# Kernel tuning notes

Hardware: AMD Instinct MI355X
Metric: run time of the kernel (lower is better)

The kernel has to match this reference:

```python
import jax, jax.numpy as jnp
import numpy as np

B, T, E, A = 4, 4096, 1024, 1024

def setup_inputs() -> dict:
    key = jax.random.key(0)
    k1, k2, k3, k4 = jax.random.split(key, 4)
    scale = 1.0 / np.sqrt(E)  # ~ nn.Linear default init scale
    return {
        "embedded": jax.random.normal(k1, (B, T, E), dtype=jnp.float32),
        "Wq": jax.random.uniform(k2, (A, E), jnp.float32, -scale, scale),
        "Wk": jax.random.uniform(k3, (A, E), jnp.float32, -scale, scale),
        "Wv": jax.random.uniform(k4, (A, E), jnp.float32, -scale, scale),
    }

def reference(embedded, Wq, Wk, Wv):
    # QKV projections (nn.Linear without bias: x @ W.T)
    q = jnp.einsum('bte,ae->bta', embedded, Wq)
    k = jnp.einsum('bte,ae->bta', embedded, Wk)
    v = jnp.einsum('bte,ae->bta', embedded, Wv)
    A_dim = q.shape[-1]
    # scaled scores [B, T, T]
    scores = jnp.einsum('bqa,bka->bqk', q, k) / jnp.sqrt(jnp.float32(A_dim))
    # causal mask (lower triangular allowed)
    Tq = scores.shape[-1]
    causal = jnp.tril(jnp.ones((Tq, Tq), dtype=bool))
    scores = jnp.where(causal, scores, -jnp.inf)
    probs = jax.nn.softmax(scores, axis=-1)
    out = jnp.einsum('bqk,bka->bqa', probs, v)
    return jnp.round(out, 4)
```

## Files before the change

### kernel.cpp

```cpp
#include <hip/hip_runtime.h>
#include <hip/hip_bf16.h>

using bf16 = __hip_bfloat16;

typedef __attribute__((ext_vector_type(4))) float f32x4;
typedef __attribute__((ext_vector_type(8))) short short8;

typedef const void __attribute__((address_space(1)))* gas1_t;
typedef void __attribute__((address_space(3)))* las3_t;
#define GLDS(gp, lp) __builtin_amdgcn_global_load_lds((gas1_t)(gp), (las3_t)(lp), 16, 0, 0)

__device__ inline short f2bfbits(float f) {
  union { bf16 h; short s; } u;
  u.h = __float2bfloat16(f);
  return u.s;
}
__device__ inline float bf2f(short u) {
  unsigned x = ((unsigned)(unsigned short)u) << 16;
  float f; __builtin_memcpy(&f, &x, 4); return f;
}

__device__ inline void store_out(float* C, size_t idx, float v) { C[idx] = v; }
__device__ inline void store_out(bf16* C, size_t idx, float v) { C[idx] = __float2bfloat16(v); }

template<typename TOUT, int MODE>
__global__ __launch_bounds__(512, 2) void gemm256(
    const short* __restrict__ A, int lda, size_t sAz,
    const short* __restrict__ B, int ldb, size_t sBz,
    TOUT* __restrict__ C, int ldc, size_t sCz,
    int K, float scale)
{
  int bx, by;
  if constexpr (MODE == 1) {
    const int i = blockIdx.x;
    by = (int)((__builtin_sqrtf(8.f * (float)i + 1.f) - 1.f) * 0.5f);
    if (((by * (by + 1)) >> 1) > i) by--;
    else if ((((by + 1) * (by + 2)) >> 1) <= i) by++;
    bx = i - ((by * (by + 1)) >> 1);
  } else {
    bx = blockIdx.x; by = blockIdx.y;
  }
  const int z = blockIdx.z;
  const int tri_by = (by * (by + 1)) >> 1;

  A += (size_t)z * sAz;
  B += (size_t)z * sBz;
  C += (size_t)z * sCz;

  const int NT = K >> 5;

  __shared__ short As[3][256 * 32];
  __shared__ short Bs[3][256 * 32];

  const int t = threadIdx.x;
  const int lane = t & 63;
  const int wave = t >> 6;
  const int wm = wave >> 2;
  const int wn = wave & 3;
  const int fr = lane & 15, kh = lane >> 4;
  const int koff = ((kh ^ ((fr >> 1) & 3)) << 3);

  int srow[2], scol[2];
  #pragma unroll
  for (int j = 0; j < 2; j++) {
    int e = j * 512 + t;
    srow[j] = e >> 2;
    scol[j] = (((e & 3) ^ ((e >> 3) & 3)) << 3);
  }

  f32x4 acc[8][4];
  #pragma unroll
  for (int i = 0; i < 8; i++)
    #pragma unroll
    for (int j = 0; j < 4; j++) acc[i][j] = (f32x4){0.f, 0.f, 0.f, 0.f};

  auto STAGE_A = [&](int kt) {
    const int buf = kt % 3, k0 = kt * 32;
    #pragma unroll
    for (int j = 0; j < 2; j++) {
      const short* pa = A + (size_t)(by * 256 + srow[j]) * lda + k0 + scol[j];
      GLDS(pa, (char*)&As[buf][0] + j * 8192 + wave * 1024);
    }
  };
  auto STAGE_B = [&](int kt) {
    const int buf = kt % 3, k0 = kt * 32;
    #pragma unroll
    for (int j = 0; j < 2; j++) {
      const short* pb = B + (size_t)(bx * 256 + srow[j]) * ldb + k0 + scol[j];
      GLDS(pb, (char*)&Bs[buf][0] + j * 8192 + wave * 1024);
    }
  };

  STAGE_A(0); STAGE_B(0);
  STAGE_A(1); STAGE_B(1);
  asm volatile("s_waitcnt vmcnt(4)\ns_barrier" ::: "memory");

  const int arow = wm * 128 + fr;
  const int brow = wn * 64 + fr;

  for (int kt = 0; kt < NT; kt++) {
    const short* as = &As[kt % 3][0];
    const short* bs = &Bs[kt % 3][0];
    short8 af[4], bfr[4];

    #pragma unroll
    for (int n = 0; n < 4; n++) bfr[n] = *(const short8*)&bs[(brow + n * 16) * 32 + koff];
    #pragma unroll
    for (int m = 0; m < 4; m++) af[m] = *(const short8*)&as[(arow + m * 16) * 32 + koff];
    if (kt + 2 < NT) STAGE_A(kt + 2);
    __builtin_amdgcn_s_barrier();
    asm volatile("s_waitcnt lgkmcnt(0)" ::: "memory");
    __builtin_amdgcn_sched_barrier(0);
    __builtin_amdgcn_s_setprio(1);
    #pragma unroll
    for (int m = 0; m < 4; m++)
      #pragma unroll
      for (int n = 0; n < 4; n++)
        acc[m][n] = __builtin_amdgcn_mfma_f32_16x16x32_bf16(af[m], bfr[n], acc[m][n], 0, 0, 0);
    __builtin_amdgcn_s_setprio(0);
    __builtin_amdgcn_sched_barrier(0);

    #pragma unroll
    for (int m = 0; m < 4; m++) af[m] = *(const short8*)&as[(arow + (m + 4) * 16) * 32 + koff];
    if (kt + 2 < NT) STAGE_B(kt + 2);
    __builtin_amdgcn_s_barrier();
    asm volatile("s_waitcnt lgkmcnt(0)" ::: "memory");
    __builtin_amdgcn_sched_barrier(0);
    __builtin_amdgcn_s_setprio(1);
    #pragma unroll
    for (int m = 0; m < 4; m++)
      #pragma unroll
      for (int n = 0; n < 4; n++)
        acc[m + 4][n] = __builtin_amdgcn_mfma_f32_16x16x32_bf16(af[m], bfr[n], acc[m + 4][n], 0, 0, 0);
    __builtin_amdgcn_s_setprio(0);
    __builtin_amdgcn_sched_barrier(0);

    if (kt + 2 < NT)      asm volatile("s_waitcnt vmcnt(4)\ns_barrier" ::: "memory");
    else if (kt + 1 < NT) asm volatile("s_waitcnt vmcnt(0)\ns_barrier" ::: "memory");
  }

  #pragma unroll
  for (int m = 0; m < 8; m++)
    #pragma unroll
    for (int n = 0; n < 4; n++) {
      int col_l = wn * 64 + n * 16 + fr;
      #pragma unroll
      for (int r = 0; r < 4; r++) {
        int row_l = wm * 128 + m * 16 + kh * 4 + r;
        if constexpr (MODE == 1)
          store_out(C, (size_t)(tri_by + bx) * 65536 + (size_t)row_l * 256 + col_l,
                    acc[m][n][r] * scale);
        else
          store_out(C, (size_t)(by * 256 + row_l) * ldc + bx * 256 + col_l,
                    acc[m][n][r] * scale);
      }
    }
}

__global__ __launch_bounds__(512, 2) void gemm_pv_split(
    const short* __restrict__ SP, const short* __restrict__ Vt,
    float* __restrict__ Out, float* __restrict__ Ppart)
{
  const int w = blockIdx.x;
  int by, bx, z, kt0, kt1, u;
  bool topart;
  if (w < 128) {
    by = w & 7; bx = (w >> 3) & 3; z = w >> 5;
    kt0 = 0; kt1 = (by + 1) * 8; topart = false; u = 0;
  } else {
    const int v = w - 128;
    const int h = v & 1;
    u = v >> 1;
    by = 8 + (u & 7); bx = (u >> 3) & 3; z = u >> 5;
    const int n = (by + 1) * 8, half = n >> 1;
    kt0 = h ? half : 0;
    kt1 = h ? n : half;
    topart = (h == 1);
  }
  const int tri_by = (by * (by + 1)) >> 1;
  const short* A = SP + (size_t)z * 136 * 65536;

  __shared__ short As[3][256 * 32];
  __shared__ short Bs[3][256 * 32];

  const int t = threadIdx.x;
  const int lane = t & 63;
  const int wave = t >> 6;
  const int wm = wave >> 2;
  const int wn = wave & 3;
  const int fr = lane & 15, kh = lane >> 4;
  const int koff = ((kh ^ ((fr >> 1) & 3)) << 3);

  int srow[2], scol[2];
  #pragma unroll
  for (int j = 0; j < 2; j++) {
    int e = j * 512 + t;
    srow[j] = e >> 2;
    scol[j] = (((e & 3) ^ ((e >> 3) & 3)) << 3);
  }

  f32x4 acc[8][4];
  #pragma unroll
  for (int i = 0; i < 8; i++)
    #pragma unroll
    for (int j = 0; j < 4; j++) acc[i][j] = (f32x4){0.f, 0.f, 0.f, 0.f};

  auto STAGE_A = [&](int kt) {
    const int buf = kt % 3, k0 = kt * 32;
    #pragma unroll
    for (int j = 0; j < 2; j++) {
      const short* pa = A + (size_t)(tri_by + (k0 >> 8)) * 65536
                          + (size_t)srow[j] * 256 + (k0 & 255) + scol[j];
      GLDS(pa, (char*)&As[buf][0] + j * 8192 + wave * 1024);
    }
  };
  auto STAGE_B = [&](int kt) {
    const int buf = kt % 3, k0 = kt * 32;
    #pragma unroll
    for (int j = 0; j < 2; j++) {
      const short* pb = Vt + (size_t)(bx * 256 + srow[j]) * 16384 + z * 4096 + k0 + scol[j];
      GLDS(pb, (char*)&Bs[buf][0] + j * 8192 + wave * 1024);
    }
  };

  STAGE_A(kt0); STAGE_B(kt0);
  STAGE_A(kt0 + 1); STAGE_B(kt0 + 1);
  asm volatile("s_waitcnt vmcnt(4)\ns_barrier" ::: "memory");

  const int arow = wm * 128 + fr;
  const int brow = wn * 64 + fr;

  for (int kt = kt0; kt < kt1; kt++) {
    const short* as = &As[kt % 3][0];
    const short* bs = &Bs[kt % 3][0];
    short8 af[4], bfr[4];

    #pragma unroll
    for (int n = 0; n < 4; n++) bfr[n] = *(const short8*)&bs[(brow + n * 16) * 32 + koff];
    #pragma unroll
    for (int m = 0; m < 4; m++) af[m] = *(const short8*)&as[(arow + m * 16) * 32 + koff];
    if (kt + 2 < kt1) STAGE_A(kt + 2);
    __builtin_amdgcn_s_barrier();
    asm volatile("s_waitcnt lgkmcnt(0)" ::: "memory");
    __builtin_amdgcn_sched_barrier(0);
    __builtin_amdgcn_s_setprio(1);
    #pragma unroll
    for (int m = 0; m < 4; m++)
      #pragma unroll
      for (int n = 0; n < 4; n++)
        acc[m][n] = __builtin_amdgcn_mfma_f32_16x16x32_bf16(af[m], bfr[n], acc[m][n], 0, 0, 0);
    __builtin_amdgcn_s_setprio(0);
    __builtin_amdgcn_sched_barrier(0);

    #pragma unroll
    for (int m = 0; m < 4; m++) af[m] = *(const short8*)&as[(arow + (m + 4) * 16) * 32 + koff];
    if (kt + 2 < kt1) STAGE_B(kt + 2);
    __builtin_amdgcn_s_barrier();
    asm volatile("s_waitcnt lgkmcnt(0)" ::: "memory");
    __builtin_amdgcn_sched_barrier(0);
    __builtin_amdgcn_s_setprio(1);
    #pragma unroll
    for (int m = 0; m < 4; m++)
      #pragma unroll
      for (int n = 0; n < 4; n++)
        acc[m + 4][n] = __builtin_amdgcn_mfma_f32_16x16x32_bf16(af[m], bfr[n], acc[m + 4][n], 0, 0, 0);
    __builtin_amdgcn_s_setprio(0);
    __builtin_amdgcn_sched_barrier(0);

    if (kt + 2 < kt1)      asm volatile("s_waitcnt vmcnt(4)\ns_barrier" ::: "memory");
    else if (kt + 1 < kt1) asm volatile("s_waitcnt vmcnt(0)\ns_barrier" ::: "memory");
  }

  #pragma unroll
  for (int m = 0; m < 8; m++)
    #pragma unroll
    for (int n = 0; n < 4; n++) {
      int col_l = wn * 64 + n * 16 + fr;
      #pragma unroll
      for (int r = 0; r < 4; r++) {
        int row_l = wm * 128 + m * 16 + kh * 4 + r;
        if (topart)
          Ppart[(size_t)u * 65536 + (size_t)row_l * 256 + col_l] = acc[m][n][r];
        else
          Out[(size_t)z * 4096 * 1024 + (size_t)(by * 256 + row_l) * 1024
              + bx * 256 + col_l] = acc[m][n][r];
      }
    }
}

__global__ __launch_bounds__(256) void pv_reduce(
    const float* __restrict__ Ppart, float* __restrict__ Out)
{
  const int u = blockIdx.x;
  const int rg = blockIdx.y;
  const int by = 8 + (u & 7), bx = (u >> 3) & 3, z = u >> 5;
  const int t = threadIdx.x;
  const float* src = Ppart + (size_t)u * 65536 + (size_t)rg * 32 * 256;
  float* dst = Out + (size_t)z * 4096 * 1024
                   + (size_t)(by * 256 + rg * 32) * 1024 + bx * 256;
  for (int i = t * 4; i < 8192; i += 1024) {
    int row = i >> 8, col = i & 255;
    f32x4 a = *(const f32x4*)&src[i];
    float* d = &dst[(size_t)row * 1024 + col];
    f32x4 b = *(const f32x4*)d;
    b[0] += a[0]; b[1] += a[1]; b[2] += a[2]; b[3] += a[3];
    *(f32x4*)d = b;
  }
}

__global__ __launch_bounds__(256) void gemm128(
    const short* __restrict__ A, int lda,
    const short* __restrict__ B, int ldb,
    bf16* __restrict__ C, int ldc, int K, float scale)
{
  const int bx = blockIdx.x, by = blockIdx.y;
  __shared__ short a_lds[128 * 32];
  __shared__ short b_lds[128 * 32];

  const int t = threadIdx.x;
  const int lane = t & 63;
  const int wave = t >> 6;
  const int wm = wave >> 1, wn = wave & 1;
  const int fr = lane & 15, kh = lane >> 4;

  f32x4 acc[4][4];
  #pragma unroll
  for (int i = 0; i < 4; i++)
    #pragma unroll
    for (int j = 0; j < 4; j++) acc[i][j] = (f32x4){0.f, 0.f, 0.f, 0.f};

  for (int k0 = 0; k0 < K; k0 += 32) {
    #pragma unroll
    for (int i = 0; i < 2; i++) {
      int e = i * 256 + t;
      int r_ = e >> 2, c_ = (e & 3) * 8;
      GLDS(A + (size_t)(by * 128 + r_) * lda + k0 + c_, (char*)a_lds + i * 4096 + wave * 1024);
      GLDS(B + (size_t)(bx * 128 + r_) * ldb + k0 + c_, (char*)b_lds + i * 4096 + wave * 1024);
    }
    __syncthreads();

    short8 af[4], bfr[4];
    #pragma unroll
    for (int m = 0; m < 4; m++)
      af[m] = *(const short8*)&a_lds[(wm * 64 + m * 16 + fr) * 32 + kh * 8];
    #pragma unroll
    for (int n = 0; n < 4; n++)
      bfr[n] = *(const short8*)&b_lds[(wn * 64 + n * 16 + fr) * 32 + kh * 8];
    #pragma unroll
    for (int m = 0; m < 4; m++)
      #pragma unroll
      for (int n = 0; n < 4; n++)
        acc[m][n] = __builtin_amdgcn_mfma_f32_16x16x32_bf16(af[m], bfr[n], acc[m][n], 0, 0, 0);
    __syncthreads();
  }

  #pragma unroll
  for (int m = 0; m < 4; m++)
    #pragma unroll
    for (int n = 0; n < 4; n++) {
      int col = bx * 128 + wn * 64 + n * 16 + fr;
      #pragma unroll
      for (int r = 0; r < 4; r++) {
        int row = by * 128 + wm * 64 + m * 16 + kh * 4 + r;
        C[(size_t)row * ldc + col] = __float2bfloat16(acc[m][n][r] * scale);
      }
    }
}

__global__ __launch_bounds__(256) void cvt_bf16(
    const float* __restrict__ in, bf16* __restrict__ out, int n, float scale)
{
  for (int i = (blockIdx.x * 256 + threadIdx.x) * 8; i < n; i += gridDim.x * 2048) {
    f32x4 v0 = *(const f32x4*)&in[i];
    f32x4 v1 = *(const f32x4*)&in[i + 4];
    short8 o = { f2bfbits(v0[0] * scale), f2bfbits(v0[1] * scale),
                 f2bfbits(v0[2] * scale), f2bfbits(v0[3] * scale),
                 f2bfbits(v1[0] * scale), f2bfbits(v1[1] * scale),
                 f2bfbits(v1[2] * scale), f2bfbits(v1[3] * scale) };
    *(short8*)&out[i] = o;
  }
}

__global__ __launch_bounds__(256) void cvt_t_bf16(
    const float* __restrict__ in, bf16* __restrict__ out, int N)
{
  __shared__ float tile[64][65];
  const int bx = blockIdx.x, by = blockIdx.y;
  const int t = threadIdx.x;
  #pragma unroll
  for (int i = 0; i < 16; i++) {
    int e = i * 256 + t;
    int r = e >> 6, c = e & 63;
    tile[r][c] = in[(size_t)(by * 64 + r) * N + bx * 64 + c];
  }
  __syncthreads();
  #pragma unroll
  for (int i = 0; i < 16; i++) {
    int e = i * 256 + t;
    int r = e >> 6, c = e & 63;
    out[(size_t)(bx * 64 + r) * N + by * 64 + c] = __float2bfloat16(tile[c][r]);
  }
}

__global__ __launch_bounds__(256) void softmax_causal_packed(short* SP, int T)
{
  __shared__ float rowv[4096];
  __shared__ float red[4];
  const int r = blockIdx.x;
  const int z = blockIdx.y;
  const int rb = r >> 8, rl = r & 255;
  const size_t tri = (size_t)((rb * (rb + 1)) >> 1);
  short* base = SP + (size_t)z * 136 * 65536;
  const int L = r + 1;
  const int kend = (rb + 1) * 256;
  const int t = threadIdx.x;

  float lmax = -3.0e38f;
  for (int i = t * 8; i < kend; i += 2048) {
    short8 s = *(const short8*)(base + (tri + (i >> 8)) * 65536 + (size_t)rl * 256 + (i & 255));
    #pragma unroll
    for (int j = 0; j < 8; j++) {
      float v = bf2f(s[j]);
      rowv[i + j] = v;
      if (i + j < L) lmax = fmaxf(lmax, v);
    }
  }
  #pragma unroll
  for (int o = 32; o > 0; o >>= 1) lmax = fmaxf(lmax, __shfl_down(lmax, o));
  if ((t & 63) == 0) red[t >> 6] = lmax;
  __syncthreads();
  const float m = fmaxf(fmaxf(red[0], red[1]), fmaxf(red[2], red[3]));
  __syncthreads();

  float lsum = 0.f;
  for (int i = t; i < kend; i += 256) {
    float e = (i < L) ? __expf(rowv[i] - m) : 0.f;
    rowv[i] = e;
    lsum += e;
  }
  #pragma unroll
  for (int o = 32; o > 0; o >>= 1) lsum += __shfl_down(lsum, o);
  if ((t & 63) == 0) red[t >> 6] = lsum;
  __syncthreads();
  const float inv = 1.f / (red[0] + red[1] + red[2] + red[3]);

  for (int i = t * 8; i < kend; i += 2048) {
    short8 o;
    #pragma unroll
    for (int j = 0; j < 8; j++) o[j] = f2bfbits(rowv[i + j] * inv);
    *(short8*)(base + (tri + (i >> 8)) * 65536 + (size_t)rl * 256 + (i & 255)) = o;
  }
}

extern "C" void kernel_launch(void* const* d_in, const int* in_sizes, int n_in,
                              void* d_out, int out_size, void* d_ws, size_t ws_size,
                              hipStream_t stream) {
  (void)in_sizes; (void)n_in; (void)out_size; (void)ws_size;
  const float* X  = (const float*)d_in[0];
  const float* Wq = (const float*)d_in[1];
  const float* Wk = (const float*)d_in[2];
  const float* Wv = (const float*)d_in[3];
  float* Out = (float*)d_out;

  const int Bn = 4, T = 4096, E = 1024, Ad = 1024;
  const int M = Bn * T;

  char* ws = (char*)d_ws;
  short* Q2  = (short*)ws;
  short* Vt  = (short*)(ws + 33554432);
  short* Xb  = (short*)(ws + 67108864);
  short* WqT = (short*)(ws + 100663296);
  short* WkT = (short*)(ws + 102760448);
  short* Wvb = (short*)(ws + 104857600);
  short* W2T = (short*)(ws + 106954752);
  short* SP  = (short*)(ws + 109051904);
  float* Ppart = (float*)ws;

  dim3 blk(256), blk5(512);
  const size_t SPz = (size_t)136 * 65536;

  cvt_bf16<<<dim3(8192), blk, 0, stream>>>(X, (bf16*)Xb, M * E, 1.0f);
  cvt_t_bf16<<<dim3(16, 16), blk, 0, stream>>>(Wq, (bf16*)WqT, E);
  cvt_t_bf16<<<dim3(16, 16), blk, 0, stream>>>(Wk, (bf16*)WkT, E);
  cvt_bf16<<<dim3(512), blk, 0, stream>>>(Wv, (bf16*)Wvb, Ad * E, 1.0f);

  gemm128<<<dim3(8, 8), blk, 0, stream>>>(
      WkT, Ad, WqT, Ad, (bf16*)W2T, E, Ad, 0.03125f);

  gemm256<bf16, 0><<<dim3(1024 / 256, M / 256), blk5, 0, stream>>>(
      Xb, E, 0, W2T, E, 0, (bf16*)Q2, 1024, 0, E, 1.0f);

  gemm256<bf16, 0><<<dim3(M / 256, Ad / 256), blk5, 0, stream>>>(
      Wvb, E, 0, Xb, E, 0, (bf16*)Vt, M, 0, E, 1.0f);

  gemm256<bf16, 1><<<dim3(136, 1, Bn), blk5, 0, stream>>>(
      Q2, 1024, (size_t)T * 1024,
      Xb, 1024, (size_t)T * 1024,
      (bf16*)SP, 256, SPz, E, 1.0f);

  softmax_causal_packed<<<dim3(T, Bn), blk, 0, stream>>>(SP, T);

  gemm_pv_split<<<dim3(384), blk5, 0, stream>>>(SP, Vt, Out, Ppart);
  pv_reduce<<<dim3(128, 8), blk, 0, stream>>>(Ppart, Out);
}
```

Before: 407.5 us.

## Rebalance causal PV GEMM work across 256 blocks and vectorize softmax exp loop

Replaces the PV split scheme (128 full blocks plus 256 half-split blocks) with 256 blocks that each get a near-equal share of causal K-tiles. Some blocks process two row tiles back to back, and the tail of long rows is written to partial buffers that the reduce kernel then adds in. The aim is to remove load imbalance and the tail effect from uneven triangular work, with fewer partial buffers to reduce. The softmax exp/sum loop also moves to 4-wide float vector LDS accesses. Risks are the added chunk loop with extra barriers and register pressure from re-initialising accumulators inside the loop.

```diff
diff --git a/kernel.cpp b/kernel.cpp
--- a/kernel.cpp
+++ b/kernel.cpp
@@ -157,28 +157,15 @@
     }
 }
 
-__global__ __launch_bounds__(512, 2) void gemm_pv_split(
+__global__ __launch_bounds__(512, 2) void gemm_pv_bal(
     const short* __restrict__ SP, const short* __restrict__ Vt,
     float* __restrict__ Out, float* __restrict__ Ppart)
 {
   const int w = blockIdx.x;
-  int by, bx, z, kt0, kt1, u;
-  bool topart;
-  if (w < 128) {
-    by = w & 7; bx = (w >> 3) & 3; z = w >> 5;
-    kt0 = 0; kt1 = (by + 1) * 8; topart = false; u = 0;
-  } else {
-    const int v = w - 128;
-    const int h = v & 1;
-    u = v >> 1;
-    by = 8 + (u & 7); bx = (u >> 3) & 3; z = u >> 5;
-    const int n = (by + 1) * 8, half = n >> 1;
-    kt0 = h ? half : 0;
-    kt1 = h ? n : half;
-    topart = (h == 1);
-  }
-  const int tri_by = (by * (by + 1)) >> 1;
-  const short* A = SP + (size_t)z * 136 * 65536;
+  const int combo = w >> 4;
+  const int slot = w & 15;
+  const int bx = combo & 3, z = combo >> 2;
+  const short* Abase = SP + (size_t)z * 136 * 65536;
 
   __shared__ short As[3][256 * 32];
   __shared__ short Bs[3][256 * 32];
@@ -198,94 +185,105 @@
     srow[j] = e >> 2;
     scol[j] = (((e & 3) ^ ((e >> 3) & 3)) << 3);
   }
-
-  f32x4 acc[8][4];
-  #pragma unroll
-  for (int i = 0; i < 8; i++)
-    #pragma unroll
-    for (int j = 0; j < 4; j++) acc[i][j] = (f32x4){0.f, 0.f, 0.f, 0.f};
-
-  auto STAGE_A = [&](int kt) {
-    const int buf = kt % 3, k0 = kt * 32;
-    #pragma unroll
-    for (int j = 0; j < 2; j++) {
-      const short* pa = A + (size_t)(tri_by + (k0 >> 8)) * 65536
-                          + (size_t)srow[j] * 256 + (k0 & 255) + scol[j];
-      GLDS(pa, (char*)&As[buf][0] + j * 8192 + wave * 1024);
-    }
-  };
-  auto STAGE_B = [&](int kt) {
-    const int buf = kt % 3, k0 = kt * 32;
-    #pragma unroll
-    for (int j = 0; j < 2; j++) {
-      const short* pb = Vt + (size_t)(bx * 256 + srow[j]) * 16384 + z * 4096 + k0 + scol[j];
-      GLDS(pb, (char*)&Bs[buf][0] + j * 8192 + wave * 1024);
-    }
-  };
-
-  STAGE_A(kt0); STAGE_B(kt0);
-  STAGE_A(kt0 + 1); STAGE_B(kt0 + 1);
-  asm volatile("s_waitcnt vmcnt(4)\ns_barrier" ::: "memory");
-
   const int arow = wm * 128 + fr;
   const int brow = wn * 64 + fr;
 
-  for (int kt = kt0; kt < kt1; kt++) {
-    const short* as = &As[kt % 3][0];
-    const short* bs = &Bs[kt % 3][0];
-    short8 af[4], bfr[4];
-
-    #pragma unroll
-    for (int n = 0; n < 4; n++) bfr[n] = *(const short8*)&bs[(brow + n * 16) * 32 + koff];
-    #pragma unroll
-    for (int m = 0; m < 4; m++) af[m] = *(const short8*)&as[(arow + m * 16) * 32 + koff];
-    if (kt + 2 < kt1) STAGE_A(kt + 2);
+  const int nchunk = (slot >= 9) ? 2 : 1;
+  for (int c = 0; c < nchunk; c++) {
+    int by, u0, u1, pp;
+    if (c == 1)            { by = slot - 9;  u0 = 0; u1 = slot - 8; pp = -1; }
+    else if (slot < 8)     { by = 8 + slot;  u0 = 0; u1 = 9;        pp = -1; }
+    else if (slot == 8)    { by = 7;         u0 = 0; u1 = 8;        pp = -1; }
+    else                   { by = 24 - slot; u0 = 9; u1 = by + 1;   pp = slot - 9; }
+    const int tri_by = (by * (by + 1)) >> 1;
+    const int kt0 = u0 * 8, kt1 = u1 * 8;
+
+    f32x4 acc[8][4];
+    #pragma unroll
+    for (int i = 0; i < 8; i++)
+      #pragma unroll
+      for (int j = 0; j < 4; j++) acc[i][j] = (f32x4){0.f, 0.f, 0.f, 0.f};
+
+    auto STAGE_A = [&](int kt) {
+      const int buf = kt % 3, k0 = kt * 32;
+      #pragma unroll
+      for (int j = 0; j < 2; j++) {
+        const short* pa = Abase + (size_t)(tri_by + (k0 >> 8)) * 65536
+                                + (size_t)srow[j] * 256 + (k0 & 255) + scol[j];
+        GLDS(pa, (char*)&As[buf][0] + j * 8192 + wave * 1024);
+      }
+    };
+    auto STAGE_B = [&](int kt) {
+      const int buf = kt % 3, k0 = kt * 32;
+      #pragma unroll
+      for (int j = 0; j < 2; j++) {
+        const short* pb = Vt + (size_t)(bx * 256 + srow[j]) * 16384 + z * 4096 + k0 + scol[j];
+        GLDS(pb, (char*)&Bs[buf][0] + j * 8192 + wave * 1024);
+      }
+    };
+
+    STAGE_A(kt0); STAGE_B(kt0);
+    STAGE_A(kt0 + 1); STAGE_B(kt0 + 1);
+    asm volatile("s_waitcnt vmcnt(4)\ns_barrier" ::: "memory");
+
+    for (int kt = kt0; kt < kt1; kt++) {
+      const short* as = &As[kt % 3][0];
+      const short* bs = &Bs[kt % 3][0];
+      short8 af[4], bfr[4];
+
+      #pragma unroll
+      for (int n = 0; n < 4; n++) bfr[n] = *(const short8*)&bs[(brow + n * 16) * 32 + koff];
+      #pragma unroll
+      for (int m = 0; m < 4; m++) af[m] = *(const short8*)&as[(arow + m * 16) * 32 + koff];
+      if (kt + 2 < kt1) STAGE_A(kt + 2);
+      __builtin_amdgcn_s_barrier();
+      asm volatile("s_waitcnt lgkmcnt(0)" ::: "memory");
+      __builtin_amdgcn_sched_barrier(0);
+      __builtin_amdgcn_s_setprio(1);
+      #pragma unroll
+      for (int m = 0; m < 4; m++)
+        #pragma unroll
+        for (int n = 0; n < 4; n++)
+          acc[m][n] = __builtin_amdgcn_mfma_f32_16x16x32_bf16(af[m], bfr[n], acc[m][n], 0, 0, 0);
+      __builtin_amdgcn_s_setprio(0);
+      __builtin_amdgcn_sched_barrier(0);
+
+      #pragma unroll
+      for (int m = 0; m < 4; m++) af[m] = *(const short8*)&as[(arow + (m + 4) * 16) * 32 + koff];
+      if (kt + 2 < kt1) STAGE_B(kt + 2);
+      __builtin_amdgcn_s_barrier();
+      asm volatile("s_waitcnt lgkmcnt(0)" ::: "memory");
+      __builtin_amdgcn_sched_barrier(0);
+      __builtin_amdgcn_s_setprio(1);
+      #pragma unroll
+      for (int m = 0; m < 4; m++)
+        #pragma unroll
+        for (int n = 0; n < 4; n++)
+          acc[m + 4][n] = __builtin_amdgcn_mfma_f32_16x16x32_bf16(af[m], bfr[n], acc[m + 4][n], 0, 0, 0);
+      __builtin_amdgcn_s_setprio(0);
+      __builtin_amdgcn_sched_barrier(0);
+
+      if (kt + 2 < kt1)      asm volatile("s_waitcnt vmcnt(4)\ns_barrier" ::: "memory");
+      else                   asm volatile("s_waitcnt vmcnt(0)\ns_barrier" ::: "memory");
+    }
+
+    #pragma unroll
+    for (int m = 0; m < 8; m++)
+      #pragma unroll
+      for (int n = 0; n < 4; n++) {
+        int col_l = wn * 64 + n * 16 + fr;
+        #pragma unroll
+        for (int r = 0; r < 4; r++) {
+          int row_l = wm * 128 + m * 16 + kh * 4 + r;
+          if (pp >= 0)
+            Ppart[(size_t)(combo * 7 + pp) * 65536 + (size_t)row_l * 256 + col_l] = acc[m][n][r];
+          else
+            Out[(size_t)z * 4096 * 1024 + (size_t)(by * 256 + row_l) * 1024
+                + bx * 256 + col_l] = acc[m][n][r];
+        }
+      }
     __builtin_amdgcn_s_barrier();
-    asm volatile("s_waitcnt lgkmcnt(0)" ::: "memory");
-    __builtin_amdgcn_sched_barrier(0);
-    __builtin_amdgcn_s_setprio(1);
-    #pragma unroll
-    for (int m = 0; m < 4; m++)
-      #pragma unroll
-      for (int n = 0; n < 4; n++)
-        acc[m][n] = __builtin_amdgcn_mfma_f32_16x16x32_bf16(af[m], bfr[n], acc[m][n], 0, 0, 0);
-    __builtin_amdgcn_s_setprio(0);
-    __builtin_amdgcn_sched_barrier(0);
-
-    #pragma unroll
-    for (int m = 0; m < 4; m++) af[m] = *(const short8*)&as[(arow + (m + 4) * 16) * 32 + koff];
-    if (kt + 2 < kt1) STAGE_B(kt + 2);
-    __builtin_amdgcn_s_barrier();
-    asm volatile("s_waitcnt lgkmcnt(0)" ::: "memory");
-    __builtin_amdgcn_sched_barrier(0);
-    __builtin_amdgcn_s_setprio(1);
-    #pragma unroll
-    for (int m = 0; m < 4; m++)
-      #pragma unroll
-      for (int n = 0; n < 4; n++)
-        acc[m + 4][n] = __builtin_amdgcn_mfma_f32_16x16x32_bf16(af[m], bfr[n], acc[m + 4][n], 0, 0, 0);
-    __builtin_amdgcn_s_setprio(0);
-    __builtin_amdgcn_sched_barrier(0);
-
-    if (kt + 2 < kt1)      asm volatile("s_waitcnt vmcnt(4)\ns_barrier" ::: "memory");
-    else if (kt + 1 < kt1) asm volatile("s_waitcnt vmcnt(0)\ns_barrier" ::: "memory");
-  }
-
-  #pragma unroll
-  for (int m = 0; m < 8; m++)
-    #pragma unroll
-    for (int n = 0; n < 4; n++) {
-      int col_l = wn * 64 + n * 16 + fr;
-      #pragma unroll
-      for (int r = 0; r < 4; r++) {
-        int row_l = wm * 128 + m * 16 + kh * 4 + r;
-        if (topart)
-          Ppart[(size_t)u * 65536 + (size_t)row_l * 256 + col_l] = acc[m][n][r];
-        else
-          Out[(size_t)z * 4096 * 1024 + (size_t)(by * 256 + row_l) * 1024
-              + bx * 256 + col_l] = acc[m][n][r];
-      }
-    }
+  }
 }
 
 __global__ __launch_bounds__(256) void pv_reduce(
@@ -293,7 +291,8 @@
 {
   const int u = blockIdx.x;
   const int rg = blockIdx.y;
-  const int by = 8 + (u & 7), bx = (u >> 3) & 3, z = u >> 5;
+  const int combo = u / 7, p = u % 7;
+  const int by = 15 - p, bx = combo & 3, z = combo >> 2;
   const int t = threadIdx.x;
   const float* src = Ppart + (size_t)u * 65536 + (size_t)rg * 32 * 256;
   float* dst = Out + (size_t)z * 4096 * 1024
@@ -433,10 +432,14 @@
   __syncthreads();
 
   float lsum = 0.f;
-  for (int i = t; i < kend; i += 256) {
-    float e = (i < L) ? __expf(rowv[i] - m) : 0.f;
-    rowv[i] = e;
-    lsum += e;
+  for (int i = t * 4; i < kend; i += 1024) {
+    f32x4 v = *(const f32x4*)&rowv[i];
+    f32x4 e;
+    #pragma unroll
+    for (int j = 0; j < 4; j++)
+      e[j] = (i + j < L) ? __expf(v[j] - m) : 0.f;
+    *(f32x4*)&rowv[i] = e;
+    lsum += e[0] + e[1] + e[2] + e[3];
   }
   #pragma unroll
   for (int o = 32; o > 0; o >>= 1) lsum += __shfl_down(lsum, o);
@@ -500,6 +503,6 @@
 
   softmax_causal_packed<<<dim3(T, Bn), blk, 0, stream>>>(SP, T);
 
-  gemm_pv_split<<<dim3(384), blk5, 0, stream>>>(SP, Vt, Out, Ppart);
-  pv_reduce<<<dim3(128, 8), blk, 0, stream>>>(Ppart, Out);
-}
+  gemm_pv_bal<<<dim3(256), blk5, 0, stream>>>(SP, Vt, Out, Ppart);
+  pv_reduce<<<dim3(112, 8), blk, 0, stream>>>(Ppart, Out);
+}
```

New measurement: 367.1 us, median of 2. -9.9%, faster.
